# Optimization experiments

Hardware: AMD Instinct MI355X
Metric: run time of the kernel (lower is better)

## Reference

```python
import jax, jax.numpy as jnp
import numpy as np

B, L, D_MODEL, N_HEADS = 2, 2048, 2048, 16
HALF = D_MODEL // 2            # 1024
HD = HALF // N_HEADS           # 64 (head dim actually used by the reshape)
SCALE = float(np.sqrt(D_MODEL / N_HEADS))  # sqrt(128), per source's self.scale
EPS = 1e-5


def setup_inputs() -> dict:
    key = jax.random.key(0)
    ks = jax.random.split(key, 12)
    s = 1.0 / np.sqrt(HALF)
    d = dict(
        x_a=jax.random.normal(ks[0], (B, L, HALF), jnp.float32),
        x_b=jax.random.normal(ks[1], (B, L, HALF), jnp.float32),
        Wq_a=jax.random.normal(ks[2], (HALF, HALF), jnp.float32) * s,
        Wq_b=jax.random.normal(ks[3], (HALF, HALF), jnp.float32) * s,
        Wk_a=jax.random.normal(ks[4], (HALF, HALF), jnp.float32) * s,
        Wk_b=jax.random.normal(ks[5], (HALF, HALF), jnp.float32) * s,
        Wv_a=jax.random.normal(ks[6], (HALF, HALF), jnp.float32) * s,
        Wv_b=jax.random.normal(ks[7], (HALF, HALF), jnp.float32) * s,
        Wo_a=jax.random.normal(ks[8], (HALF, HALF), jnp.float32) * s,
        Wo_b=jax.random.normal(ks[9], (HALF, HALF), jnp.float32) * s,
        gamma_a=jnp.ones((HALF,), jnp.float32),
        beta_a=jnp.zeros((HALF,), jnp.float32),
        gamma_b=jnp.ones((HALF,), jnp.float32),
        beta_b=jnp.zeros((HALF,), jnp.float32),
    )
    return d


def _heads(x, W):
    # torch Linear (no bias): x @ W.T, then split heads -> (B, H, L, HD)
    y = jnp.einsum('bld,ed->ble', x, W)
    Bb, Ll, _ = y.shape
    return y.reshape(Bb, Ll, N_HEADS, HD).transpose(0, 2, 1, 3)


def _ln(x, gamma, beta):
    mu = jnp.mean(x, axis=-1, keepdims=True)
    var = jnp.var(x, axis=-1, keepdims=True)
    return (x - mu) * jax.lax.rsqrt(var + EPS) * gamma + beta


def reference(x_a, x_b, Wq_a, Wq_b, Wk_a, Wk_b, Wv_a, Wv_b, Wo_a, Wo_b,
              gamma_a, beta_a, gamma_b, beta_b):
    q_a = _heads(x_a, Wq_a); k_a = _heads(x_a, Wk_a); v_a = _heads(x_a, Wv_a)
    q_b = _heads(x_b, Wq_b); k_b = _heads(x_b, Wk_b); v_b = _heads(x_b, Wv_b)

    # cross-attention: branch a attends over branch b and vice versa
    scores_a = jnp.einsum('bhqd,bhkd->bhqk', q_a, k_b) / SCALE
    scores_b = jnp.einsum('bhqd,bhkd->bhqk', q_b, k_a) / SCALE
    w_a = jax.nn.softmax(scores_a, axis=-1)
    w_b = jax.nn.softmax(scores_b, axis=-1)

    o_a = jnp.einsum('bhqk,bhkd->bhqd', w_a, v_b)
    o_b = jnp.einsum('bhqk,bhkd->bhqd', w_b, v_a)
    o_a = o_a.transpose(0, 2, 1, 3).reshape(x_a.shape)
    o_b = o_b.transpose(0, 2, 1, 3).reshape(x_b.shape)

    o_a = jnp.einsum('bld,ed->ble', o_a, Wo_a)
    o_b = jnp.einsum('bld,ed->ble', o_b, Wo_b)

    y_a = _ln(x_a + o_a, gamma_a, beta_a)
    y_b = _ln(x_b + o_b, gamma_b, beta_b)
    return y_a, y_b
```

## Files before the change

### kernel.cpp

```cpp
#include <hip/hip_runtime.h>
#include <cstdint>
#include <cstddef>

typedef __bf16 bf16x8 __attribute__((ext_vector_type(8)));
typedef float f32x4 __attribute__((ext_vector_type(4)));
typedef unsigned short u16x8 __attribute__((ext_vector_type(8)));
typedef unsigned short u16x4 __attribute__((ext_vector_type(4)));
typedef unsigned short u16;

#define L_SEQ 2048
#define D_HALF 1024
#define HDIM 64
static constexpr float EXP2_SCALE = 0.12751742552639395f;

__device__ inline u16 f2b(float f) {
  uint32_t u; __builtin_memcpy(&u, &f, 4);
  u = u + 0x7FFFu + ((u >> 16) & 1u);
  return (u16)(u >> 16);
}

__global__ __launch_bounds__(256)
void convx(const float* xa, const float* xb, u16* dst) {
  const float* s = blockIdx.y ? xb : xa;
  size_t i = ((size_t)blockIdx.x * 256 + threadIdx.x) * 8;
  float4 v0 = *(const float4*)(s + i);
  float4 v1 = *(const float4*)(s + i + 4);
  u16x8 p;
  p[0] = f2b(v0.x); p[1] = f2b(v0.y); p[2] = f2b(v0.z); p[3] = f2b(v0.w);
  p[4] = f2b(v1.x); p[5] = f2b(v1.y); p[6] = f2b(v1.z); p[7] = f2b(v1.w);
  *(u16x8*)&dst[(size_t)blockIdx.y * 4194304 + i] = p;
}

struct CArg8 { const float* src[8]; };
__global__ __launch_bounds__(256)
void convw8(CArg8 a, u16* dst) {
  const int z = blockIdx.y;
  const float* s = a.src[z];
  size_t i = ((size_t)blockIdx.x * 256 + threadIdx.x) * 8;
  float4 v0 = *(const float4*)(s + i);
  float4 v1 = *(const float4*)(s + i + 4);
  u16x8 p;
  p[0] = f2b(v0.x); p[1] = f2b(v0.y); p[2] = f2b(v0.z); p[3] = f2b(v0.w);
  p[4] = f2b(v1.x); p[5] = f2b(v1.y); p[6] = f2b(v1.z); p[7] = f2b(v1.w);
  *(u16x8*)&dst[(size_t)z * 1048576 + i] = p;
}

struct GArg { const u16* A; const u16* W; u16* C; const float* R; float* Z; int vt; };
struct GArgs { GArg g[6]; };

template <bool RESID>
__global__ __launch_bounds__(256, 2)
void gemm_nt(GArgs args, int M, int N, int K) {
  GArg ga = args.g[blockIdx.z];
  __shared__ __attribute__((aligned(16))) u16 As[128][72];
  __shared__ __attribute__((aligned(16))) u16 Bs[128][72];

  const int tid = threadIdx.x;
  const int wv = tid >> 6, lane = tid & 63;
  const int lane15 = lane & 15, quad = lane >> 4;
  const int m0 = blockIdx.y * 128, n0 = blockIdx.x * 128;
  const int wm = (wv >> 1) * 64, wn = (wv & 1) * 64;

  int rr[4], cc[4];
#pragma unroll
  for (int i = 0; i < 4; i++) { int c = tid + i * 256; rr[i] = c >> 3; cc[i] = (c & 7) * 8; }

  u16x8 ra[4], rb[4];
#pragma unroll
  for (int i = 0; i < 4; i++) {
    ra[i] = *(const u16x8*)&ga.A[(size_t)(m0 + rr[i]) * K + cc[i]];
    rb[i] = *(const u16x8*)&ga.W[(size_t)(n0 + rr[i]) * K + cc[i]];
  }

  f32x4 acc[4][4] = {};

  for (int k0 = 0; k0 < K; k0 += 64) {
    __syncthreads();
#pragma unroll
    for (int i = 0; i < 4; i++) {
      *(u16x8*)&As[rr[i]][cc[i]] = ra[i];
      *(u16x8*)&Bs[rr[i]][cc[i]] = rb[i];
    }
    if (k0 + 64 < K) {
#pragma unroll
      for (int i = 0; i < 4; i++) {
        ra[i] = *(const u16x8*)&ga.A[(size_t)(m0 + rr[i]) * K + k0 + 64 + cc[i]];
        rb[i] = *(const u16x8*)&ga.W[(size_t)(n0 + rr[i]) * K + k0 + 64 + cc[i]];
      }
    }
    __syncthreads();
#pragma unroll
    for (int kk = 0; kk < 64; kk += 32) {
      bf16x8 af[4], bw[4];
#pragma unroll
      for (int i = 0; i < 4; i++)
        af[i] = *(const bf16x8*)&As[wm + i * 16 + lane15][kk + quad * 8];
#pragma unroll
      for (int j = 0; j < 4; j++)
        bw[j] = *(const bf16x8*)&Bs[wn + j * 16 + lane15][kk + quad * 8];
#pragma unroll
      for (int i = 0; i < 4; i++)
#pragma unroll
        for (int j = 0; j < 4; j++)
          acc[i][j] = __builtin_amdgcn_mfma_f32_16x16x32_bf16(af[i], bw[j], acc[i][j], 0, 0, 0);
    }
  }

  if (!RESID && ga.vt) {
#pragma unroll
    for (int i = 0; i < 4; i++)
#pragma unroll
      for (int j = 0; j < 4; j++) {
        int gm0 = m0 + wm + i * 16 + quad * 4;
        int gn  = n0 + wn + j * 16 + lane15;
        int bb = gm0 >> 11, t = gm0 & 2047;
        u16x4 pk;
#pragma unroll
        for (int r = 0; r < 4; r++) pk[r] = f2b(acc[i][j][r]);
        *(u16x4*)&ga.C[(size_t)bb * 2097152 + (size_t)gn * 2048 + t] = pk;
      }
  } else {
#pragma unroll
    for (int i = 0; i < 4; i++)
#pragma unroll
      for (int j = 0; j < 4; j++)
#pragma unroll
        for (int r = 0; r < 4; r++) {
          int gm = m0 + wm + i * 16 + quad * 4 + r;
          int gn = n0 + wn + j * 16 + lane15;
          size_t idx = (size_t)gm * N + gn;
          if (RESID) ga.Z[idx] = acc[i][j][r] + ga.R[idx];
          else       ga.C[idx] = f2b(acc[i][j][r]);
        }
  }
}

__global__ __launch_bounds__(256, 2)
void attn_kernel(const u16* q_a, const u16* k_a, const u16* vt_a,
                 const u16* q_b, const u16* k_b, const u16* vt_b,
                 u16* o_a, u16* o_b) {
  const int br = blockIdx.z;
  const u16* Q  = br ? q_b : q_a;
  const u16* Kp = br ? k_a : k_b;
  const u16* Vp = br ? vt_a : vt_b;
  u16* O = br ? o_b : o_a;
  const int bh = blockIdx.y;
  const int b = bh >> 4, h = bh & 15;
  const int q0 = blockIdx.x * 64;

  const int tid = threadIdx.x, wv = tid >> 6, lane = tid & 63;
  const int lane15 = lane & 15, quad = lane >> 4;

  __shared__ __attribute__((aligned(16))) u16 Ks[2][64][72];
  __shared__ __attribute__((aligned(16))) u16 Vt[2][64][72];
  __shared__ __attribute__((aligned(16))) u16 Pw[4][16][68];

  const size_t base   = ((size_t)b * L_SEQ) * D_HALF + (size_t)h * HDIM;
  const size_t vbase  = (size_t)b * 2097152 + (size_t)(h * 64) * 2048;

  const int c1 = tid + 256;
  const int r0 = tid >> 3, cb0 = (tid & 7) * 8;
  const int r1 = c1 >> 3,  cb1 = (c1 & 7) * 8;

  const int qrow = q0 + wv * 16 + lane15;
  bf16x8 qf0 = *(const bf16x8*)&Q[base + (size_t)qrow * D_HALF + quad * 8];
  bf16x8 qf1 = *(const bf16x8*)&Q[base + (size_t)qrow * D_HALF + 32 + quad * 8];

  u16x8 kr0 = *(const u16x8*)&Kp[base + (size_t)r0 * D_HALF + cb0];
  u16x8 kr1 = *(const u16x8*)&Kp[base + (size_t)r1 * D_HALF + cb1];
  u16x8 vr0 = *(const u16x8*)&Vp[vbase + (size_t)r0 * 2048 + cb0];
  u16x8 vr1 = *(const u16x8*)&Vp[vbase + (size_t)r1 * 2048 + cb1];
  *(u16x8*)&Ks[0][r0][cb0] = kr0;
  *(u16x8*)&Ks[0][r1][cb1] = kr1;
  *(u16x8*)&Vt[0][r0][cb0] = vr0;
  *(u16x8*)&Vt[0][r1][cb1] = vr1;
  __syncthreads();

  f32x4 oacc[4] = {};
  float l_r[4] = {0.f, 0.f, 0.f, 0.f};

  for (int it = 0; it < 32; it++) {
    const int cur = it & 1, nxt = cur ^ 1;
    if (it < 31) {
      const int kt = (it + 1) * 64;
      kr0 = *(const u16x8*)&Kp[base + (size_t)(kt + r0) * D_HALF + cb0];
      kr1 = *(const u16x8*)&Kp[base + (size_t)(kt + r1) * D_HALF + cb1];
      vr0 = *(const u16x8*)&Vp[vbase + (size_t)r0 * 2048 + kt + cb0];
      vr1 = *(const u16x8*)&Vp[vbase + (size_t)r1 * 2048 + kt + cb1];
    }

    f32x4 s[4];
#pragma unroll
    for (int nt = 0; nt < 4; nt++) {
      bf16x8 kb0 = *(const bf16x8*)&Ks[cur][nt * 16 + lane15][quad * 8];
      bf16x8 kb1 = *(const bf16x8*)&Ks[cur][nt * 16 + lane15][32 + quad * 8];
      f32x4 a0 = {};
      a0 = __builtin_amdgcn_mfma_f32_16x16x32_bf16(qf0, kb0, a0, 0, 0, 0);
      a0 = __builtin_amdgcn_mfma_f32_16x16x32_bf16(qf1, kb1, a0, 0, 0, 0);
      s[nt] = a0;
    }
#pragma unroll
    for (int nt = 0; nt < 4; nt++)
#pragma unroll
      for (int r = 0; r < 4; r++) {
        float p = __builtin_amdgcn_exp2f(s[nt][r] * EXP2_SCALE);
        s[nt][r] = p;
        l_r[r] += p;
      }

#pragma unroll
    for (int nt = 0; nt < 4; nt++)
#pragma unroll
      for (int r = 0; r < 4; r++)
        Pw[wv][quad * 4 + r][nt * 16 + lane15] = f2b(s[nt][r]);

    __asm__ volatile("s_waitcnt lgkmcnt(0)" ::: "memory");

    union { u16x4 h[2]; bf16x8 v; } up0, up1;
    up0.h[0] = *(const u16x4*)&Pw[wv][lane15][quad * 8];
    up0.h[1] = *(const u16x4*)&Pw[wv][lane15][quad * 8 + 4];
    up1.h[0] = *(const u16x4*)&Pw[wv][lane15][32 + quad * 8];
    up1.h[1] = *(const u16x4*)&Pw[wv][lane15][32 + quad * 8 + 4];
    bf16x8 pa0 = up0.v, pa1 = up1.v;

#pragma unroll
    for (int dt = 0; dt < 4; dt++) {
      bf16x8 bv0 = *(const bf16x8*)&Vt[cur][dt * 16 + lane15][quad * 8];
      bf16x8 bv1 = *(const bf16x8*)&Vt[cur][dt * 16 + lane15][32 + quad * 8];
      f32x4 t = oacc[dt];
      t = __builtin_amdgcn_mfma_f32_16x16x32_bf16(pa0, bv0, t, 0, 0, 0);
      t = __builtin_amdgcn_mfma_f32_16x16x32_bf16(pa1, bv1, t, 0, 0, 0);
      oacc[dt] = t;
    }

    if (it < 31) {
      *(u16x8*)&Ks[nxt][r0][cb0] = kr0;
      *(u16x8*)&Ks[nxt][r1][cb1] = kr1;
      *(u16x8*)&Vt[nxt][r0][cb0] = vr0;
      *(u16x8*)&Vt[nxt][r1][cb1] = vr1;
    }
    __syncthreads();
  }

  float linv[4];
#pragma unroll
  for (int r = 0; r < 4; r++) {
    float l = l_r[r];
    l += __shfl_xor(l, 1); l += __shfl_xor(l, 2);
    l += __shfl_xor(l, 4); l += __shfl_xor(l, 8);
    linv[r] = 1.0f / l;
  }
#pragma unroll
  for (int dt = 0; dt < 4; dt++)
#pragma unroll
    for (int r = 0; r < 4; r++) {
      float val = oacc[dt][r] * linv[r];
      O[base + (size_t)(q0 + wv * 16 + quad * 4 + r) * D_HALF + dt * 16 + lane15] = f2b(val);
    }
}

__global__ __launch_bounds__(256)
void ln_kernel(const float* zA, const float* zB,
               const float* gA, const float* bA, const float* gB, const float* bB,
               float* out) {
  const int row = blockIdx.x, br = blockIdx.y;
  const float* z = (br ? zB : zA) + (size_t)row * D_HALF;
  const float* g  = br ? gB : gA;
  const float* be = br ? bB : bA;
  float* o = out + (size_t)br * ((size_t)4096 * D_HALF) + (size_t)row * D_HALF;

  float4 v = ((const float4*)z)[threadIdx.x];
  float s  = v.x + v.y + v.z + v.w;
  float s2 = v.x * v.x + v.y * v.y + v.z * v.z + v.w * v.w;
#pragma unroll
  for (int off = 32; off > 0; off >>= 1) {
    s  += __shfl_down(s, off);
    s2 += __shfl_down(s2, off);
  }
  __shared__ float red[8];
  int w = threadIdx.x >> 6, ln = threadIdx.x & 63;
  if (ln == 0) { red[w] = s; red[4 + w] = s2; }
  __syncthreads();
  if (threadIdx.x == 0) {
    red[0] = red[0] + red[1] + red[2] + red[3];
    red[4] = red[4] + red[5] + red[6] + red[7];
  }
  __syncthreads();
  float mu  = red[0] * (1.0f / 1024.0f);
  float var = red[4] * (1.0f / 1024.0f) - mu * mu;
  float rs  = rsqrtf(fmaxf(var, 0.0f) + 1e-5f);

  int col = threadIdx.x * 4;
  float4 gv = ((const float4*)g)[threadIdx.x];
  float4 bv = ((const float4*)be)[threadIdx.x];
  float4 ov;
  ov.x = (v.x - mu) * rs * gv.x + bv.x;
  ov.y = (v.y - mu) * rs * gv.y + bv.y;
  ov.z = (v.z - mu) * rs * gv.z + bv.z;
  ov.w = (v.w - mu) * rs * gv.w + bv.w;
  *(float4*)&o[col] = ov;
}

extern "C" void kernel_launch(void* const* d_in, const int* in_sizes, int n_in,
                              void* d_out, int out_size, void* d_ws, size_t ws_size,
                              hipStream_t stream) {
  const float* x_a     = (const float*)d_in[0];
  const float* x_b     = (const float*)d_in[1];
  const float* Wq_a    = (const float*)d_in[2];
  const float* Wq_b    = (const float*)d_in[3];
  const float* Wk_a    = (const float*)d_in[4];
  const float* Wk_b    = (const float*)d_in[5];
  const float* Wv_a    = (const float*)d_in[6];
  const float* Wv_b    = (const float*)d_in[7];
  const float* Wo_a    = (const float*)d_in[8];
  const float* Wo_b    = (const float*)d_in[9];
  const float* gamma_a = (const float*)d_in[10];
  const float* beta_a  = (const float*)d_in[11];
  const float* gamma_b = (const float*)d_in[12];
  const float* beta_b  = (const float*)d_in[13];

  const size_t BUF = (size_t)4096 * 1024;
  u16* ws   = (u16*)d_ws;
  u16* q_a  = ws + 0 * BUF; u16* k_a  = ws + 1 * BUF; u16* vt_a = ws + 2 * BUF;
  u16* q_b  = ws + 3 * BUF; u16* k_b  = ws + 4 * BUF; u16* vt_b = ws + 5 * BUF;
  u16* wall = ws + 6 * BUF;
  float* z_a = (float*)(ws + 0 * BUF);
  float* z_b = (float*)(ws + 2 * BUF);

  u16* xbf_a = (u16*)d_out;
  u16* xbf_b = xbf_a + 4194304;
  u16* o_a   = (u16*)d_out;
  u16* o_b   = o_a + 4194304;

  const int M = 4096, N = 1024, K = 1024;

  convx<<<dim3(2048, 2), 256, 0, stream>>>(x_a, x_b, xbf_a);

  CArg8 cw;
  cw.src[0] = Wq_a; cw.src[1] = Wk_a; cw.src[2] = Wv_a;
  cw.src[3] = Wq_b; cw.src[4] = Wk_b; cw.src[5] = Wv_b;
  cw.src[6] = Wo_a; cw.src[7] = Wo_b;
  convw8<<<dim3(512, 8), 256, 0, stream>>>(cw, wall);

  GArgs qkv;
  qkv.g[0] = GArg{xbf_a, wall + 0 * 1048576, q_a,  nullptr, nullptr, 0};
  qkv.g[1] = GArg{xbf_a, wall + 1 * 1048576, k_a,  nullptr, nullptr, 0};
  qkv.g[2] = GArg{xbf_a, wall + 2 * 1048576, vt_a, nullptr, nullptr, 1};
  qkv.g[3] = GArg{xbf_b, wall + 3 * 1048576, q_b,  nullptr, nullptr, 0};
  qkv.g[4] = GArg{xbf_b, wall + 4 * 1048576, k_b,  nullptr, nullptr, 0};
  qkv.g[5] = GArg{xbf_b, wall + 5 * 1048576, vt_b, nullptr, nullptr, 1};
  gemm_nt<false><<<dim3(8, 32, 6), 256, 0, stream>>>(qkv, M, N, K);

  attn_kernel<<<dim3(32, 32, 2), 256, 0, stream>>>(q_a, k_a, vt_a, q_b, k_b, vt_b, o_a, o_b);

  GArgs op;
  op.g[0] = GArg{o_a, wall + 6 * 1048576, nullptr, x_a, z_a, 0};
  op.g[1] = GArg{o_b, wall + 7 * 1048576, nullptr, x_b, z_b, 0};
  op.g[2] = op.g[0]; op.g[3] = op.g[0]; op.g[4] = op.g[0]; op.g[5] = op.g[0];
  gemm_nt<true><<<dim3(8, 32, 2), 256, 0, stream>>>(op, M, N, K);

  ln_kernel<<<dim3(4096, 2), 256, 0, stream>>>(z_a, z_b, gamma_a, beta_a,
                                               gamma_b, beta_b, (float*)d_out);
}
```

Baseline: 378.6 us.

## Process 128 queries per attention block and keep P in registers via transposed MFMA

Each wave now handles two 16-row query fragments, so every K/V tile loaded into shared memory is reused across twice as many queries and the grid is halved. The QK^T MFMA operands are swapped so the score layout matches the A-operand layout of the 16x16x16 bf16 MFMA. This lets the softmax probabilities feed the PV product directly from registers instead of round-tripping through LDS, and a packed bf16 convert instruction is used. The cost is more registers per thread, possible occupancy loss, and fewer blocks to fill the device.

```diff
diff --git a/kernel.cpp b/kernel.cpp
--- a/kernel.cpp
+++ b/kernel.cpp
@@ -6,6 +6,7 @@
 typedef float f32x4 __attribute__((ext_vector_type(4)));
 typedef unsigned short u16x8 __attribute__((ext_vector_type(8)));
 typedef unsigned short u16x4 __attribute__((ext_vector_type(4)));
+typedef short s16x4 __attribute__((ext_vector_type(4)));
 typedef unsigned short u16;
 
 #define L_SEQ 2048
@@ -17,6 +18,12 @@
   uint32_t u; __builtin_memcpy(&u, &f, 4);
   u = u + 0x7FFFu + ((u >> 16) & 1u);
   return (u16)(u >> 16);
+}
+
+__device__ inline uint32_t cvt_pk_bf16(float lo, float hi) {
+  uint32_t r;
+  asm("v_cvt_pk_bf16_f32 %0, %1, %2" : "=v"(r) : "v"(lo), "v"(hi));
+  return r;
 }
 
 __global__ __launch_bounds__(256)
@@ -135,6 +142,12 @@
   }
 }
 
+#if __has_builtin(__builtin_amdgcn_mfma_f32_16x16x16bf16_1k)
+#define HAVE_MFMA16 1
+#else
+#define HAVE_MFMA16 0
+#endif
+
 __global__ __launch_bounds__(256, 2)
 void attn_kernel(const u16* q_a, const u16* k_a, const u16* vt_a,
                  const u16* q_b, const u16* k_b, const u16* vt_b,
@@ -146,14 +159,16 @@
   u16* O = br ? o_b : o_a;
   const int bh = blockIdx.y;
   const int b = bh >> 4, h = bh & 15;
-  const int q0 = blockIdx.x * 64;
+  const int q0 = blockIdx.x * 128;
 
   const int tid = threadIdx.x, wv = tid >> 6, lane = tid & 63;
   const int lane15 = lane & 15, quad = lane >> 4;
 
   __shared__ __attribute__((aligned(16))) u16 Ks[2][64][72];
   __shared__ __attribute__((aligned(16))) u16 Vt[2][64][72];
-  __shared__ __attribute__((aligned(16))) u16 Pw[4][16][68];
+#if !HAVE_MFMA16
+  __shared__ __attribute__((aligned(16))) u16 Pw[4][2][16][72];
+#endif
 
   const size_t base   = ((size_t)b * L_SEQ) * D_HALF + (size_t)h * HDIM;
   const size_t vbase  = (size_t)b * 2097152 + (size_t)(h * 64) * 2048;
@@ -162,9 +177,14 @@
   const int r0 = tid >> 3, cb0 = (tid & 7) * 8;
   const int r1 = c1 >> 3,  cb1 = (c1 & 7) * 8;
 
-  const int qrow = q0 + wv * 16 + lane15;
-  bf16x8 qf0 = *(const bf16x8*)&Q[base + (size_t)qrow * D_HALF + quad * 8];
-  bf16x8 qf1 = *(const bf16x8*)&Q[base + (size_t)qrow * D_HALF + 32 + quad * 8];
+  bf16x8 qf[2][2];
+#pragma unroll
+  for (int f = 0; f < 2; f++) {
+    const int qrow = q0 + wv * 32 + f * 16 + lane15;
+#pragma unroll
+    for (int c = 0; c < 2; c++)
+      qf[f][c] = *(const bf16x8*)&Q[base + (size_t)qrow * D_HALF + c * 32 + quad * 8];
+  }
 
   u16x8 kr0 = *(const u16x8*)&Kp[base + (size_t)r0 * D_HALF + cb0];
   u16x8 kr1 = *(const u16x8*)&Kp[base + (size_t)r1 * D_HALF + cb1];
@@ -176,8 +196,8 @@
   *(u16x8*)&Vt[0][r1][cb1] = vr1;
   __syncthreads();
 
-  f32x4 oacc[4] = {};
-  float l_r[4] = {0.f, 0.f, 0.f, 0.f};
+  f32x4 oacc[2][4] = {};
+  float lsum[2] = {0.f, 0.f};
 
   for (int it = 0; it < 32; it++) {
     const int cur = it & 1, nxt = cur ^ 1;
@@ -189,49 +209,79 @@
       vr1 = *(const u16x8*)&Vp[vbase + (size_t)r1 * 2048 + kt + cb1];
     }
 
-    f32x4 s[4];
+    f32x4 s[2][4];
 #pragma unroll
     for (int nt = 0; nt < 4; nt++) {
       bf16x8 kb0 = *(const bf16x8*)&Ks[cur][nt * 16 + lane15][quad * 8];
       bf16x8 kb1 = *(const bf16x8*)&Ks[cur][nt * 16 + lane15][32 + quad * 8];
-      f32x4 a0 = {};
-      a0 = __builtin_amdgcn_mfma_f32_16x16x32_bf16(qf0, kb0, a0, 0, 0, 0);
-      a0 = __builtin_amdgcn_mfma_f32_16x16x32_bf16(qf1, kb1, a0, 0, 0, 0);
-      s[nt] = a0;
-    }
-#pragma unroll
-    for (int nt = 0; nt < 4; nt++)
-#pragma unroll
-      for (int r = 0; r < 4; r++) {
-        float p = __builtin_amdgcn_exp2f(s[nt][r] * EXP2_SCALE);
-        s[nt][r] = p;
-        l_r[r] += p;
-      }
-
-#pragma unroll
-    for (int nt = 0; nt < 4; nt++)
-#pragma unroll
-      for (int r = 0; r < 4; r++)
-        Pw[wv][quad * 4 + r][nt * 16 + lane15] = f2b(s[nt][r]);
-
+#pragma unroll
+      for (int f = 0; f < 2; f++) {
+        f32x4 a0 = {};
+        a0 = __builtin_amdgcn_mfma_f32_16x16x32_bf16(kb0, qf[f][0], a0, 0, 0, 0);
+        a0 = __builtin_amdgcn_mfma_f32_16x16x32_bf16(kb1, qf[f][1], a0, 0, 0, 0);
+        s[f][nt] = a0;
+      }
+    }
+
+    s16x4 pa[2][4];
+#pragma unroll
+    for (int f = 0; f < 2; f++)
+#pragma unroll
+      for (int nt = 0; nt < 4; nt++) {
+        float p0 = __builtin_amdgcn_exp2f(s[f][nt][0] * EXP2_SCALE);
+        float p1 = __builtin_amdgcn_exp2f(s[f][nt][1] * EXP2_SCALE);
+        float p2 = __builtin_amdgcn_exp2f(s[f][nt][2] * EXP2_SCALE);
+        float p3 = __builtin_amdgcn_exp2f(s[f][nt][3] * EXP2_SCALE);
+        lsum[f] += (p0 + p1) + (p2 + p3);
+        union { uint32_t u[2]; s16x4 v; } cv;
+        cv.u[0] = cvt_pk_bf16(p0, p1);
+        cv.u[1] = cvt_pk_bf16(p2, p3);
+        pa[f][nt] = cv.v;
+      }
+
+#if HAVE_MFMA16
+#pragma unroll
+    for (int dt = 0; dt < 4; dt++) {
+      s16x4 bv[4];
+#pragma unroll
+      for (int nt = 0; nt < 4; nt++)
+        bv[nt] = *(const s16x4*)&Vt[cur][dt * 16 + lane15][nt * 16 + quad * 4];
+#pragma unroll
+      for (int f = 0; f < 2; f++) {
+        f32x4 t = oacc[f][dt];
+#pragma unroll
+        for (int nt = 0; nt < 4; nt++)
+          t = __builtin_amdgcn_mfma_f32_16x16x16bf16_1k(pa[f][nt], bv[nt], t, 0, 0, 0);
+        oacc[f][dt] = t;
+      }
+    }
+#else
+#pragma unroll
+    for (int f = 0; f < 2; f++)
+#pragma unroll
+      for (int nt = 0; nt < 4; nt++)
+        *(s16x4*)&Pw[wv][f][lane15][nt * 16 + quad * 4] = pa[f][nt];
     __asm__ volatile("s_waitcnt lgkmcnt(0)" ::: "memory");
-
-    union { u16x4 h[2]; bf16x8 v; } up0, up1;
-    up0.h[0] = *(const u16x4*)&Pw[wv][lane15][quad * 8];
-    up0.h[1] = *(const u16x4*)&Pw[wv][lane15][quad * 8 + 4];
-    up1.h[0] = *(const u16x4*)&Pw[wv][lane15][32 + quad * 8];
-    up1.h[1] = *(const u16x4*)&Pw[wv][lane15][32 + quad * 8 + 4];
-    bf16x8 pa0 = up0.v, pa1 = up1.v;
-
+    bf16x8 pb[2][2];
+#pragma unroll
+    for (int f = 0; f < 2; f++) {
+      pb[f][0] = *(const bf16x8*)&Pw[wv][f][lane15][quad * 8];
+      pb[f][1] = *(const bf16x8*)&Pw[wv][f][lane15][32 + quad * 8];
+    }
 #pragma unroll
     for (int dt = 0; dt < 4; dt++) {
       bf16x8 bv0 = *(const bf16x8*)&Vt[cur][dt * 16 + lane15][quad * 8];
       bf16x8 bv1 = *(const bf16x8*)&Vt[cur][dt * 16 + lane15][32 + quad * 8];
-      f32x4 t = oacc[dt];
-      t = __builtin_amdgcn_mfma_f32_16x16x32_bf16(pa0, bv0, t, 0, 0, 0);
-      t = __builtin_amdgcn_mfma_f32_16x16x32_bf16(pa1, bv1, t, 0, 0, 0);
-      oacc[dt] = t;
-    }
+#pragma unroll
+      for (int f = 0; f < 2; f++) {
+        f32x4 t = oacc[f][dt];
+        t = __builtin_amdgcn_mfma_f32_16x16x32_bf16(pb[f][0], bv0, t, 0, 0, 0);
+        t = __builtin_amdgcn_mfma_f32_16x16x32_bf16(pb[f][1], bv1, t, 0, 0, 0);
+        oacc[f][dt] = t;
+      }
+    }
+    __asm__ volatile("" ::: "memory");
+#endif
 
     if (it < 31) {
       *(u16x8*)&Ks[nxt][r0][cb0] = kr0;
@@ -242,21 +292,28 @@
     __syncthreads();
   }
 
-  float linv[4];
-#pragma unroll
-  for (int r = 0; r < 4; r++) {
-    float l = l_r[r];
-    l += __shfl_xor(l, 1); l += __shfl_xor(l, 2);
-    l += __shfl_xor(l, 4); l += __shfl_xor(l, 8);
-    linv[r] = 1.0f / l;
-  }
-#pragma unroll
-  for (int dt = 0; dt < 4; dt++)
-#pragma unroll
-    for (int r = 0; r < 4; r++) {
-      float val = oacc[dt][r] * linv[r];
-      O[base + (size_t)(q0 + wv * 16 + quad * 4 + r) * D_HALF + dt * 16 + lane15] = f2b(val);
-    }
+#pragma unroll
+  for (int f = 0; f < 2; f++) {
+    float lt = lsum[f];
+    lt += __shfl_xor(lt, 16);
+    lt += __shfl_xor(lt, 32);
+    lsum[f] = lt;
+  }
+#pragma unroll
+  for (int f = 0; f < 2; f++) {
+    float linv[4];
+#pragma unroll
+    for (int r = 0; r < 4; r++)
+      linv[r] = 1.0f / __shfl(lsum[f], quad * 4 + r);
+#pragma unroll
+    for (int dt = 0; dt < 4; dt++)
+#pragma unroll
+      for (int r = 0; r < 4; r++) {
+        float val = oacc[f][dt][r] * linv[r];
+        O[base + (size_t)(q0 + wv * 32 + f * 16 + quad * 4 + r) * D_HALF
+          + dt * 16 + lane15] = f2b(val);
+      }
+  }
 }
 
 __global__ __launch_bounds__(256)
@@ -351,7 +408,7 @@
   qkv.g[5] = GArg{xbf_b, wall + 5 * 1048576, vt_b, nullptr, nullptr, 1};
   gemm_nt<false><<<dim3(8, 32, 6), 256, 0, stream>>>(qkv, M, N, K);
 
-  attn_kernel<<<dim3(32, 32, 2), 256, 0, stream>>>(q_a, k_a, vt_a, q_b, k_b, vt_b, o_a, o_b);
+  attn_kernel<<<dim3(16, 32, 2), 256, 0, stream>>>(q_a, k_a, vt_a, q_b, k_b, vt_b, o_a, o_b);
 
   GArgs op;
   op.g[0] = GArg{o_a, wall + 6 * 1048576, nullptr, x_a, z_a, 0};
```

New measurement: 341.6 us. -9.8%, faster.
